# Optimization experiments

Measured on AMD Instinct MI355X. Metric: run time of the kernel, lower is better.

The kernel has to match this reference:

```python
import jax, jax.numpy as jnp
import numpy as np


def setup_inputs() -> dict:
    key = jax.random.key(0)
    kq, kk, kv = jax.random.split(key, 3)
    B, S, D = 4, 4096, 128
    q = jax.random.normal(kq, (B, S, D), dtype=jnp.float32)
    k = jax.random.normal(kk, (B, S, D), dtype=jnp.float32)
    v = jax.random.normal(kv, (B, S, D), dtype=jnp.float32)
    return {"q": q, "k": k, "v": v}


def reference(q, k, v):
    # naive scaled dot-product attention: softmax(q k^T / sqrt(d)) v
    scale = 1.0 / jnp.sqrt(jnp.asarray(q.shape[-1], q.dtype))
    scores = jnp.einsum("bsd,btd->bst", q, k) * scale  # [B,S,S]
    probs = jax.nn.softmax(scores, axis=-1)
    out = jnp.einsum("bst,btd->bsd", probs, v)  # [B,S,Dv]
    return out
```

## Files before the change

kernel.cpp:

```cpp
#include <hip/hip_runtime.h>
#include <cmath>
#include <cstdint>

typedef __attribute__((ext_vector_type(8))) __bf16 bf16x8;
typedef __attribute__((ext_vector_type(16))) float f32x16;
typedef unsigned int u32;
typedef unsigned short u16;

constexpr int Bn = 4, Sn = 4096, Dn = 128;
constexpr int OSTR = 132;
constexpr float SCL2E = 0.08838834764831845f * 1.4426950408889634f;

__device__ __forceinline__ u32 pk2(float a, float b) {
  u32 ua = __builtin_bit_cast(u32, a) + 0x8000u;
  u32 ub = __builtin_bit_cast(u32, b) + 0x8000u;
  return __builtin_amdgcn_perm(ub, ua, 0x07060302u);
}

__launch_bounds__(256, 2)
__global__ void prep_kv(const float* __restrict__ Kg, const float* __restrict__ Vg,
                        u16* __restrict__ Kf, u16* __restrict__ Vf) {
  __shared__ float Tl[64 * 132];
  const int kt = blockIdx.x, b = blockIdx.y;
  const int tid = threadIdx.x;
  const size_t tileBase = ((size_t)b * 64 + kt) * 1024;
  const bool isV = blockIdx.z != 0;
  const float* src = (isV ? Vg : Kg) + ((size_t)b * Sn + kt * 64) * Dn;

  #pragma unroll
  for (int r = 0; r < 8; ++r) {
    const int idx = tid + r * 256;
    const int row = idx >> 5, col = (idx & 31) * 4;
    *(float4*)(Tl + row * 132 + col) = *(const float4*)(src + (size_t)row * Dn + col);
  }
  __syncthreads();

  if (!isV) {
    #pragma unroll
    for (int r = 0; r < 4; ++r) {
      const int g = tid + r * 256;
      const int c = g & 31, h = (g >> 5) & 1, tile = (g >> 6) & 1, kc = g >> 7;
      const float* p = Tl + (tile * 32 + c) * 132 + kc * 16 + h * 8;
      uint4 o;
      o.x = pk2(p[0], p[1]); o.y = pk2(p[2], p[3]);
      o.z = pk2(p[4], p[5]); o.w = pk2(p[6], p[7]);
      *(uint4*)(Kf + (tileBase + g) * 8) = o;
    }
  } else {
    #pragma unroll
    for (int r = 0; r < 4; ++r) {
      const int g = tid + r * 256;
      const int c = g & 31, h = (g >> 5) & 1, nt = (g >> 6) & 3, kc2 = g >> 8;
      const int key0 = kc2 * 16 + h * 8, dcol = nt * 32 + c;
      float x[8];
      #pragma unroll
      for (int j = 0; j < 8; ++j) x[j] = Tl[(key0 + j) * 132 + dcol];
      uint4 o;
      o.x = pk2(x[0], x[1]); o.y = pk2(x[2], x[3]);
      o.z = pk2(x[4], x[5]); o.w = pk2(x[6], x[7]);
      *(uint4*)(Vf + (tileBase + g) * 8) = o;
    }
  }
}

__launch_bounds__(256, 2)
__global__ void attn_mfma(const float* __restrict__ qg, const u16* __restrict__ Kf,
                          const u16* __restrict__ Vf, float* __restrict__ Og) {
  __shared__ __align__(16) unsigned char lds[68608];
  float* Oc = (float*)lds;
  float* ml = (float*)(lds + 67584);

  const int tid = threadIdx.x;
  const int kp = tid >> 6, lane = tid & 63;
  const int c = lane & 31, h = lane >> 5;
  const int b = blockIdx.x & 3;
  const int q0 = (blockIdx.x >> 2) * 32;

  const u16* Kb = Kf + ((size_t)b * 64) * 1024 * 8;
  const u16* Vb = Vf + ((size_t)b * 64) * 1024 * 8;

  bf16x8 qf[8];
  {
    const float* Qr = qg + ((size_t)b * Sn + q0 + c) * Dn;
    #pragma unroll
    for (int kc = 0; kc < 8; ++kc) {
      float4 f0 = *(const float4*)(Qr + kc * 16 + h * 8);
      float4 f1 = *(const float4*)(Qr + kc * 16 + h * 8 + 4);
      uint4 t;
      t.x = pk2(f0.x * SCL2E, f0.y * SCL2E);
      t.y = pk2(f0.z * SCL2E, f0.w * SCL2E);
      t.z = pk2(f1.x * SCL2E, f1.y * SCL2E);
      t.w = pk2(f1.z * SCL2E, f1.w * SCL2E);
      qf[kc] = __builtin_bit_cast(bf16x8, t);
    }
  }

  f32x16 accO[4];
  #pragma unroll
  for (int nt = 0; nt < 4; ++nt)
    #pragma unroll
    for (int r = 0; r < 16; ++r) accO[nt][r] = 0.f;
  float l_i = 0.f;

  #pragma unroll 2
  for (int t8 = 0; t8 < 16; ++t8) {
    const int kt = kp * 16 + t8;
    const u16* Kt = Kb + (size_t)kt * 1024 * 8;
    const u16* Vt = Vb + (size_t)kt * 1024 * 8;

    f32x16 sa0, sa1;
    #pragma unroll
    for (int r = 0; r < 16; ++r) { sa0[r] = 0.f; sa1[r] = 0.f; }
    #pragma unroll
    for (int kc = 0; kc < 8; ++kc) {
      uint4 a0 = *(const uint4*)(Kt + (size_t)((kc * 4 + 0 + h) * 32 + c) * 8);
      uint4 a1 = *(const uint4*)(Kt + (size_t)((kc * 4 + 2 + h) * 32 + c) * 8);
      sa0 = __builtin_amdgcn_mfma_f32_32x32x16_bf16(__builtin_bit_cast(bf16x8, a0), qf[kc], sa0, 0, 0, 0);
      sa1 = __builtin_amdgcn_mfma_f32_32x32x16_bf16(__builtin_bit_cast(bf16x8, a1), qf[kc], sa1, 0, 0, 0);
    }

    float rs = 0.f;
    #pragma unroll
    for (int r = 0; r < 16; ++r) { sa0[r] = exp2f(sa0[r]); rs += sa0[r]; }
    #pragma unroll
    for (int r = 0; r < 16; ++r) { sa1[r] = exp2f(sa1[r]); rs += sa1[r]; }
    rs += __shfl_xor(rs, 32);
    l_i += rs;

    u32 pk2v[2][8];
    #pragma unroll
    for (int i = 0; i < 8; ++i) {
      pk2v[0][i] = pk2(sa0[2 * i], sa0[2 * i + 1]);
      pk2v[1][i] = pk2(sa1[2 * i], sa1[2 * i + 1]);
    }

    #pragma unroll
    for (int kc2 = 0; kc2 < 4; ++kc2) {
      const int t = kc2 >> 1;
      const int bb = (kc2 & 1) * 4;
      u32 o0 = pk2v[t][bb], o1 = pk2v[t][bb + 1], o2 = pk2v[t][bb + 2], o3 = pk2v[t][bb + 3];
      u32 r0 = (u32)__shfl_xor((int)o0, 32);
      u32 r1 = (u32)__shfl_xor((int)o1, 32);
      u32 r2 = (u32)__shfl_xor((int)o2, 32);
      u32 r3 = (u32)__shfl_xor((int)o3, 32);
      uint4 afi;
      afi.x = h ? r2 : o0;
      afi.y = h ? r3 : o1;
      afi.z = h ? o2 : r0;
      afi.w = h ? o3 : r1;
      bf16x8 af = __builtin_bit_cast(bf16x8, afi);
      #pragma unroll
      for (int nt = 0; nt < 4; ++nt) {
        uint4 av = *(const uint4*)(Vt + (size_t)((kc2 * 8 + nt * 2 + h) * 32 + c) * 8);
        accO[nt] = __builtin_amdgcn_mfma_f32_32x32x16_bf16(__builtin_bit_cast(bf16x8, av), af, accO[nt], 0, 0, 0);
      }
    }
  }

  __syncthreads();
  {
    float* od = Oc + (size_t)(kp * 32) * OSTR;
    #pragma unroll
    for (int nt = 0; nt < 4; ++nt)
      #pragma unroll
      for (int r = 0; r < 16; ++r) {
        const int dr = (r & 3) + 8 * (r >> 2) + 4 * h;
        od[c * OSTR + nt * 32 + dr] = accO[nt][r];
      }
    if (h == 0) ml[kp * 32 + c] = l_i;
  }
  __syncthreads();
  {
    const int row = tid >> 3;
    const int d0 = (tid & 7) * 16;
    float lsum = 0.f;
    #pragma unroll
    for (int k2 = 0; k2 < 4; ++k2) lsum += ml[k2 * 32 + row];
    const float inv = 1.f / lsum;
    float4 acc[4];
    #pragma unroll
    for (int j = 0; j < 4; ++j) acc[j] = float4{0.f, 0.f, 0.f, 0.f};
    #pragma unroll
    for (int k2 = 0; k2 < 4; ++k2) {
      const float* oc = Oc + (size_t)(k2 * 32 + row) * OSTR + d0;
      #pragma unroll
      for (int j = 0; j < 4; ++j) {
        float4 vv = *(const float4*)(oc + 4 * j);
        acc[j].x += vv.x; acc[j].y += vv.y;
        acc[j].z += vv.z; acc[j].w += vv.w;
      }
    }
    float* op = Og + ((size_t)b * Sn + q0 + row) * Dn + d0;
    #pragma unroll
    for (int j = 0; j < 4; ++j) {
      float4 o = {acc[j].x * inv, acc[j].y * inv, acc[j].z * inv, acc[j].w * inv};
      *(float4*)(op + 4 * j) = o;
    }
  }
}

extern "C" void kernel_launch(void* const* d_in, const int* in_sizes, int n_in,
                              void* d_out, int out_size, void* d_ws, size_t ws_size,
                              hipStream_t stream) {
  const float* q = (const float*)d_in[0];
  const float* k = (const float*)d_in[1];
  const float* v = (const float*)d_in[2];
  float* out = (float*)d_out;
  const size_t N = (size_t)Bn * Sn * Dn;
  u16* Kf = (u16*)d_ws;
  u16* Vf = Kf + N;

  prep_kv<<<dim3(Sn / 64, Bn, 2), dim3(256), 0, stream>>>(k, v, Kf, Vf);
  attn_mfma<<<dim3((Sn / 32) * Bn), dim3(256), 0, stream>>>(q, Kf, Vf, out);
}
```

Baseline: 127.9 us.

## Split key range across eight waves and reduce partial outputs in chunks

Each block now runs 512 threads, so eight waves each handle eight key tiles instead of four waves handling sixteen. The final cross-wave reduction stages partial outputs through a smaller padded LDS buffer one 32-column chunk at a time. The goal is more waves per block to hide latency, plus smaller LDS use for higher occupancy. In exchange the reduction needs more barriers and narrower stores, and the launch bound of four blocks per CU may force register spills.

```diff
diff --git a/kernel.cpp b/kernel.cpp
--- a/kernel.cpp
+++ b/kernel.cpp
@@ -8,7 +8,6 @@
 typedef unsigned short u16;
 
 constexpr int Bn = 4, Sn = 4096, Dn = 128;
-constexpr int OSTR = 132;
 constexpr float SCL2E = 0.08838834764831845f * 1.4426950408889634f;
 
 __device__ __forceinline__ u32 pk2(float a, float b) {
@@ -63,12 +62,11 @@
   }
 }
 
-__launch_bounds__(256, 2)
+__launch_bounds__(512, 4)
 __global__ void attn_mfma(const float* __restrict__ qg, const u16* __restrict__ Kf,
                           const u16* __restrict__ Vf, float* __restrict__ Og) {
-  __shared__ __align__(16) unsigned char lds[68608];
-  float* Oc = (float*)lds;
-  float* ml = (float*)(lds + 67584);
+  __shared__ __align__(16) float Ob[8 * 32 * 33];
+  __shared__ float ml[8 * 32];
 
   const int tid = threadIdx.x;
   const int kp = tid >> 6, lane = tid & 63;
@@ -102,9 +100,9 @@
     for (int r = 0; r < 16; ++r) accO[nt][r] = 0.f;
   float l_i = 0.f;
 
-  #pragma unroll 2
-  for (int t8 = 0; t8 < 16; ++t8) {
-    const int kt = kp * 16 + t8;
+  #pragma unroll 1
+  for (int t8 = 0; t8 < 8; ++t8) {
+    const int kt = kp * 8 + t8;
     const u16* Kt = Kb + (size_t)kt * 1024 * 8;
     const u16* Vt = Vb + (size_t)kt * 1024 * 8;
 
@@ -157,45 +155,37 @@
     }
   }
 
+  if (h == 0) ml[kp * 32 + c] = l_i;
   __syncthreads();
-  {
-    float* od = Oc + (size_t)(kp * 32) * OSTR;
-    #pragma unroll
-    for (int nt = 0; nt < 4; ++nt)
+  const int qq = (tid >> 4) & 31;
+  const int dp = (tid & 15) * 2;
+  float lsum = 0.f;
+  #pragma unroll
+  for (int w2 = 0; w2 < 8; ++w2) lsum += ml[w2 * 32 + qq];
+  const float inv = 1.f / lsum;
+
+  #pragma unroll
+  for (int nt = 0; nt < 4; ++nt) {
+    if (nt) __syncthreads();
+    {
+      float* od = Ob + kp * (32 * 33) + c * 33;
       #pragma unroll
       for (int r = 0; r < 16; ++r) {
         const int dr = (r & 3) + 8 * (r >> 2) + 4 * h;
-        od[c * OSTR + nt * 32 + dr] = accO[nt][r];
+        od[dr] = accO[nt][r];
       }
-    if (h == 0) ml[kp * 32 + c] = l_i;
-  }
-  __syncthreads();
-  {
-    const int row = tid >> 3;
-    const int d0 = (tid & 7) * 16;
-    float lsum = 0.f;
-    #pragma unroll
-    for (int k2 = 0; k2 < 4; ++k2) lsum += ml[k2 * 32 + row];
-    const float inv = 1.f / lsum;
-    float4 acc[4];
-    #pragma unroll
-    for (int j = 0; j < 4; ++j) acc[j] = float4{0.f, 0.f, 0.f, 0.f};
-    #pragma unroll
-    for (int k2 = 0; k2 < 4; ++k2) {
-      const float* oc = Oc + (size_t)(k2 * 32 + row) * OSTR + d0;
-      #pragma unroll
-      for (int j = 0; j < 4; ++j) {
-        float4 vv = *(const float4*)(oc + 4 * j);
-        acc[j].x += vv.x; acc[j].y += vv.y;
-        acc[j].z += vv.z; acc[j].w += vv.w;
-      }
-    }
-    float* op = Og + ((size_t)b * Sn + q0 + row) * Dn + d0;
-    #pragma unroll
-    for (int j = 0; j < 4; ++j) {
-      float4 o = {acc[j].x * inv, acc[j].y * inv, acc[j].z * inv, acc[j].w * inv};
-      *(float4*)(op + 4 * j) = o;
-    }
+    }
+    __syncthreads();
+    float s0 = 0.f, s1 = 0.f;
+    #pragma unroll
+    for (int w2 = 0; w2 < 8; ++w2) {
+      const float* ob = Ob + w2 * (32 * 33) + qq * 33 + dp;
+      s0 += ob[0];
+      s1 += ob[1];
+    }
+    float* op = Og + ((size_t)b * Sn + q0 + qq) * Dn + nt * 32 + dp;
+    op[0] = s0 * inv;
+    op[1] = s1 * inv;
   }
 }
 
@@ -211,5 +201,5 @@
   u16* Vf = Kf + N;
 
   prep_kv<<<dim3(Sn / 64, Bn, 2), dim3(256), 0, stream>>>(k, v, Kf, Vf);
-  attn_mfma<<<dim3((Sn / 32) * Bn), dim3(256), 0, stream>>>(q, Kf, Vf, out);
-}
+  attn_mfma<<<dim3((Sn / 32) * Bn), dim3(512), 0, stream>>>(q, Kf, Vf, out);
+}
```

Result: slower. 214.0 us (+67.3%).
